# Optimization experiments

Measured on AMD Instinct MI355X. Metric: run time of the kernel, lower is better.

Reference implementation:

```python
import jax, jax.numpy as jnp
import numpy as np

D = 1024
H = 4096  # int(dim * mlp_ratio)
E = 8
B, N = 2, 2048


def setup_inputs() -> dict:
    key = jax.random.key(0)
    ks = jax.random.split(key, 5)
    x = jax.random.normal(ks[0], (B, N, D), dtype=jnp.float32)
    # torch Linear weights, stored pre-transposed for right-multiplication
    W1 = jax.random.normal(ks[1], (E, D, H), dtype=jnp.float32) / np.sqrt(D)
    W2 = jax.random.normal(ks[2], (E, H, D), dtype=jnp.float32) / np.sqrt(H)
    Wg = jax.random.normal(ks[3], (D, E), dtype=jnp.float32) / np.sqrt(D)
    bg = jax.random.normal(ks[4], (E,), dtype=jnp.float32) * 0.01
    return {"x": x, "W1": W1, "W2": W2, "Wg": Wg, "bg": bg}


def reference(x, W1, W2, Wg, bg):
    b, n, d = x.shape
    e = Wg.shape[1]
    xf = x.reshape(b * n, d)                      # [T, D]
    logits = xf @ Wg + bg                         # [T, E]
    one_hot = jax.nn.one_hot(jnp.argmax(logits, axis=-1), e, dtype=x.dtype)  # [T, E]
    # Dense all-experts compute (faithful to the original module)
    h = jax.nn.gelu(jnp.einsum('td,edh->eth', xf, W1), approximate=True)     # [E, T, H]
    y = jnp.einsum('eth,ehd->etd', h, W2)                                    # [E, T, D]
    out = jnp.einsum('etd,te->td', y, one_hot)                               # top-1 combine
    return out.reshape(b, n, d)
```

## Files before the change

kernel.cpp:

```cpp
#include <hip/hip_runtime.h>
#include <hip/hip_bf16.h>

#define Dq 1024
#define Hq 4096
#define Tq 4096
#define MAXTILES 40

#define XB_OFF 65536
#define HC_OFF (XB_OFF + Tq * Dq * 2)

#define M_NT 0
#define M_CNT 8
#define M_POFF 16
#define M_CUR 32
#define M_TE 64
#define M_TR 128
#define M_EXP 512
#define M_PERM 4608

typedef __attribute__((ext_vector_type(8))) short bf16x8;
typedef __attribute__((ext_vector_type(4))) float f32x4;

__device__ __forceinline__ short f2bf(float f) {
    __hip_bfloat16 h = __float2bfloat16(f);
    return *reinterpret_cast<short*>(&h);
}

__device__ __forceinline__ float gelu_tanh(float x) {
    float u = 0.7978845608028654f * (x + 0.044715f * x * x * x);
    return x / (1.0f + __expf(-2.0f * u));
}

typedef __attribute__((address_space(1))) const void gvoid;
typedef __attribute__((address_space(3))) void lvoid;
__device__ __forceinline__ void glds16(const void* g, void* l) {
    __builtin_amdgcn_global_load_lds((gvoid*)g, (lvoid*)l, 16, 0, 0);
}

#define WAITVM_(N) asm volatile("s_waitcnt vmcnt(" #N ")" ::: "memory")
#define WAITVM(N) WAITVM_(N)

__global__ void k_init(int* meta) {
    int i = blockIdx.x * 256 + threadIdx.x;
    if (i < M_PERM + MAXTILES * 128) meta[i] = 0;
}

__global__ void k_route(const float* __restrict__ x, const float* __restrict__ Wg,
                        const float* __restrict__ bg, int* meta, short* __restrict__ xb) {
    int wave = threadIdx.x >> 6;
    int lane = threadIdx.x & 63;
    int t = blockIdx.x * 4 + wave;
    const float* xr = x + (size_t)t * Dq;
    float acc[8];
#pragma unroll
    for (int e = 0; e < 8; ++e) acc[e] = 0.0f;
#pragma unroll
    for (int j = 0; j < 16; ++j) {
        int d = j * 64 + lane;
        float xv = xr[d];
        xb[(size_t)t * Dq + d] = f2bf(xv);
        float4 w0 = *(const float4*)(Wg + (size_t)d * 8);
        float4 w1 = *(const float4*)(Wg + (size_t)d * 8 + 4);
        acc[0] += xv * w0.x; acc[1] += xv * w0.y; acc[2] += xv * w0.z; acc[3] += xv * w0.w;
        acc[4] += xv * w1.x; acc[5] += xv * w1.y; acc[6] += xv * w1.z; acc[7] += xv * w1.w;
    }
#pragma unroll
    for (int e = 0; e < 8; ++e) {
#pragma unroll
        for (int off = 32; off > 0; off >>= 1) acc[e] += __shfl_xor(acc[e], off);
    }
    if (lane == 0) {
        float best = acc[0] + bg[0];
        int be = 0;
#pragma unroll
        for (int e = 1; e < 8; ++e) {
            float v = acc[e] + bg[e];
            if (v > best) { best = v; be = e; }
        }
        meta[M_EXP + t] = be;
        atomicAdd(&meta[M_CNT + be], 1);
    }
}

__global__ void k_scan(int* meta) {
    if (threadIdx.x != 0) return;
    int off = 0, nt = 0;
    for (int e = 0; e < 8; ++e) {
        meta[M_POFF + e] = off;
        int c = meta[M_CNT + e];
        int m = (c + 127) / 128;
        for (int j = 0; j < m; ++j) {
            meta[M_TE + nt] = e;
            meta[M_TR + nt] = off + j * 128;
            ++nt;
        }
        off += m * 128;
    }
    meta[M_POFF + 8] = off;
    meta[M_NT] = nt;
}

__global__ void k_scatter(int* meta) {
    int t = blockIdx.x * 256 + threadIdx.x;
    if (t >= Tq) return;
    int e = meta[M_EXP + t];
    int pos = atomicAdd(&meta[M_CUR + e], 1);
    meta[M_PERM + meta[M_POFF + e] + pos] = t;
}

#define STEP(RC, RN, P, ISS, KN, LDB)                                          \
  {                                                                            \
    if (ISS) {                                                                 \
      _Pragma("unroll")                                                        \
      for (int s = 0; s < 4; ++s)                                              \
        glds16(aSrc[s] + (size_t)(KN) * 64, As + (1 - (P)) * 8192 + ldsA[s]);  \
      _Pragma("unroll")                                                        \
      for (int r = 0; r < 8; ++r)                                              \
        RN[r] = *(const float4*)(bSrc + ((size_t)(KN) * 64 + r) * (LDB));      \
      WAITVM(12);                                                              \
    } else {                                                                   \
      WAITVM(0);                                                               \
    }                                                                          \
    _Pragma("unroll")                                                          \
    for (int j = 0; j < 4; ++j) {                                              \
      bf16x8 v;                                                                \
      _Pragma("unroll")                                                        \
      for (int r = 0; r < 8; ++r) v[r] = f2bf(((const float*)&RC[r])[j]);      \
      *(bf16x8*)(Bs + (P) * 8192 + bwoff[j]) = v;                              \
    }                                                                          \
    asm volatile("s_waitcnt lgkmcnt(0)" ::: "memory");                         \
    __builtin_amdgcn_s_barrier();                                              \
    asm volatile("" ::: "memory");                                             \
    __builtin_amdgcn_sched_barrier(0);                                         \
    _Pragma("unroll")                                                          \
    for (int s2 = 0; s2 < 2; ++s2) {                                           \
      bf16x8 af[4], bfv[4];                                                    \
      _Pragma("unroll")                                                        \
      for (int f = 0; f < 4; ++f) {                                            \
        af[f]  = *(const bf16x8*)(&As[(P) * 8192 + aoff[s2][f]]);              \
        bfv[f] = *(const bf16x8*)(&Bs[(P) * 8192 + boff[s2][f]]);              \
      }                                                                        \
      __builtin_amdgcn_s_setprio(1);                                           \
      _Pragma("unroll")                                                        \
      for (int fm = 0; fm < 4; ++fm)                                           \
        _Pragma("unroll")                                                      \
        for (int fn = 0; fn < 4; ++fn)                                         \
          acc[fm][fn] = __builtin_amdgcn_mfma_f32_16x16x32_bf16(               \
              af[fm], bfv[fn], acc[fm][fn], 0, 0, 0);                          \
      __builtin_amdgcn_s_setprio(0);                                           \
    }                                                                          \
    __builtin_amdgcn_s_barrier();                                              \
    asm volatile("" ::: "memory");                                             \
  }

#define GEMM_SETUP()                                                           \
    int tt = threadIdx.x, w = tt >> 6, lane = tt & 63;                         \
    int fr = lane & 15, fg = lane >> 4;                                        \
    int rlo = lane >> 3, csw = (lane & 7) ^ rlo;                               \
    int ldsA[4];                                                               \
    _Pragma("unroll")                                                          \
    for (int s = 0; s < 4; ++s) ldsA[s] = (s * 32 + w * 8) * 64;               \
    int n4 = (tt & 31) * 4, kb = (tt >> 5) * 8;                                \
    int bwoff[4];                                                              \
    _Pragma("unroll")                                                          \
    for (int j = 0; j < 4; ++j) {                                              \
      int n = n4 + j;                                                          \
      bwoff[j] = n * 64 + (((kb >> 3) ^ ((n + (n >> 3)) & 7)) * 8);            \
    }                                                                          \
    int wm = (w >> 1) * 64, wn = (w & 1) * 64;                                 \
    int aoff[2][4], boff[2][4];                                                \
    _Pragma("unroll")                                                          \
    for (int s2 = 0; s2 < 2; ++s2)                                             \
      _Pragma("unroll")                                                        \
      for (int f = 0; f < 4; ++f) {                                            \
        int c = s2 * 4 + fg;                                                   \
        int m = wm + f * 16 + fr;                                              \
        aoff[s2][f] = m * 64 + ((c ^ (m & 7)) * 8);                            \
        int n = wn + f * 16 + fr;                                              \
        boff[s2][f] = n * 64 + ((c ^ ((n + (n >> 3)) & 7)) * 8);               \
      }                                                                        \
    f32x4 acc[4][4];                                                           \
    _Pragma("unroll")                                                          \
    for (int a = 0; a < 4; ++a)                                                \
      _Pragma("unroll")                                                        \
      for (int b = 0; b < 4; ++b) acc[a][b] = (f32x4){0.f, 0.f, 0.f, 0.f};

__global__ __launch_bounds__(256, 2) void k_gemm1(const short* __restrict__ xb,
                                                  const float* __restrict__ W1,
                                                  const int* __restrict__ meta,
                                                  short* __restrict__ Hc) {
    __shared__ short As[2 * 128 * 64];
    __shared__ short Bs[2 * 128 * 64];
    int hw = blockIdx.x;
    int swzid = (hw & 7) * 160 + (hw >> 3);
    int q = swzid % 160;
    int mt = q >> 2;
    int n0 = ((swzid / 160) * 4 + (q & 3)) * 128;
    if (mt >= meta[M_NT]) return;
    int e = meta[M_TE + mt];
    int i0 = meta[M_TR + mt];
    const int* perm = meta + M_PERM;

    GEMM_SETUP()

    const short* aSrc[4];
#pragma unroll
    for (int s = 0; s < 4; ++s) {
        int row = s * 32 + w * 8 + rlo;
        aSrc[s] = xb + (size_t)perm[i0 + row] * Dq + csw * 8;
    }
    const float* bSrc = W1 + ((size_t)e * Dq + kb) * Hq + n0 + n4;

    float4 rB0[8], rB1[8];
#pragma unroll
    for (int s = 0; s < 4; ++s) glds16(aSrc[s], As + ldsA[s]);
#pragma unroll
    for (int r = 0; r < 8; ++r) rB0[r] = *(const float4*)(bSrc + (size_t)r * Hq);

    for (int t = 0; t < 16; t += 2) {
        STEP(rB0, rB1, 0, true, t + 1, Hq)
        STEP(rB1, rB0, 1, (t + 2) < 16, t + 2, Hq)
    }

#pragma unroll
    for (int fm = 0; fm < 4; ++fm) {
        int rbase = i0 + wm + fm * 16 + fg * 4;
#pragma unroll
        for (int fn = 0; fn < 4; ++fn) {
            int col = n0 + wn + fn * 16 + fr;
#pragma unroll
            for (int p = 0; p < 4; ++p) {
                float v = gelu_tanh(acc[fm][fn][p]);
                Hc[(size_t)(rbase + p) * Hq + col] = f2bf(v);
            }
        }
    }
}

__global__ __launch_bounds__(256, 2) void k_gemm2(const short* __restrict__ Hc,
                                                  const float* __restrict__ W2,
                                                  const int* __restrict__ meta,
                                                  float* __restrict__ out) {
    __shared__ short As[2 * 128 * 64];
    __shared__ short Bs[2 * 128 * 64];
    int hw = blockIdx.x;
    int swzid = (hw & 7) * 80 + (hw >> 3);
    int q = swzid % 80;
    int mt = q >> 1;
    int kbase = (q & 1) * (Hq / 2);
    int n0 = (swzid / 80) * 128;
    if (mt >= meta[M_NT]) return;
    int e = meta[M_TE + mt];
    int i0 = meta[M_TR + mt];
    const int* perm = meta + M_PERM;
    int vend = meta[M_POFF + e] + meta[M_CNT + e];

    GEMM_SETUP()

    const short* aSrc[4];
#pragma unroll
    for (int s = 0; s < 4; ++s) {
        int row = s * 32 + w * 8 + rlo;
        aSrc[s] = Hc + (size_t)(i0 + row) * Hq + kbase + csw * 8;
    }
    const float* bSrc = W2 + ((size_t)e * Hq + kbase + kb) * Dq + n0 + n4;

    float4 rB0[8], rB1[8];
#pragma unroll
    for (int s = 0; s < 4; ++s) glds16(aSrc[s], As + ldsA[s]);
#pragma unroll
    for (int r = 0; r < 8; ++r) rB0[r] = *(const float4*)(bSrc + (size_t)r * Dq);

    for (int t = 0; t < 32; t += 2) {
        STEP(rB0, rB1, 0, true, t + 1, Dq)
        STEP(rB1, rB0, 1, (t + 2) < 32, t + 2, Dq)
    }

#pragma unroll
    for (int fm = 0; fm < 4; ++fm) {
        int rbase = i0 + wm + fm * 16 + fg * 4;
#pragma unroll
        for (int p = 0; p < 4; ++p) {
            int i = rbase + p;
            if (i < vend) {
                int tok = perm[i];
#pragma unroll
                for (int fn = 0; fn < 4; ++fn) {
                    int col = n0 + wn + fn * 16 + fr;
                    atomicAdd(&out[(size_t)tok * Dq + col], acc[fm][fn][p]);
                }
            }
        }
    }
}

extern "C" void kernel_launch(void* const* d_in, const int* in_sizes, int n_in,
                              void* d_out, int out_size, void* d_ws, size_t ws_size,
                              hipStream_t stream) {
    const float* x  = (const float*)d_in[0];
    const float* W1 = (const float*)d_in[1];
    const float* W2 = (const float*)d_in[2];
    const float* Wg = (const float*)d_in[3];
    const float* bg = (const float*)d_in[4];
    float* out = (float*)d_out;
    int* meta = (int*)d_ws;
    short* xb = (short*)((char*)d_ws + XB_OFF);
    short* Hc = (short*)((char*)d_ws + HC_OFF);

    k_init<<<38, 256, 0, stream>>>(meta);
    hipMemsetAsync(d_out, 0, (size_t)Tq * Dq * 4, stream);
    k_route<<<Tq / 4, 256, 0, stream>>>(x, Wg, bg, meta, xb);
    k_scan<<<1, 64, 0, stream>>>(meta);
    k_scatter<<<Tq / 256, 256, 0, stream>>>(meta);
    k_gemm1<<<1280, 256, 0, stream>>>(xb, W1, meta, Hc);
    k_gemm2<<<640, 256, 0, stream>>>(Hc, W2, meta, out);
}
```

Before: 286.3 us.

## Pre-transpose weights to bf16 and load both GEMM operands directly to LDS

Adds a transpose kernel that converts W1 and W2 from fp32 into K-contiguous bf16 layouts in a workspace before each GEMM. Both GEMMs then fetch A and B through global-to-LDS loads with a single-buffered LDS and a simpler swizzle, dropping the in-register fp32-to-bf16 conversion of B. Occupancy hint rises to 3 and gemm2 switches to 4-way split-K over 1280 blocks. The transposes add a full extra pass over the weights each call, and the extra split-K increases atomic traffic to the output.

```diff
diff --git a/kernel.cpp b/kernel.cpp
--- a/kernel.cpp
+++ b/kernel.cpp
@@ -5,9 +5,11 @@
 #define Hq 4096
 #define Tq 4096
 #define MAXTILES 40
+#define NSTEP 16
 
 #define XB_OFF 65536
 #define HC_OFF (XB_OFF + Tq * Dq * 2)
+#define WT_OFF (HC_OFF + MAXTILES * 128 * Hq * 2)
 
 #define M_NT 0
 #define M_CNT 8
@@ -37,12 +39,36 @@
     __builtin_amdgcn_global_load_lds((gvoid*)g, (lvoid*)l, 16, 0, 0);
 }
 
-#define WAITVM_(N) asm volatile("s_waitcnt vmcnt(" #N ")" ::: "memory")
-#define WAITVM(N) WAITVM_(N)
-
 __global__ void k_init(int* meta) {
     int i = blockIdx.x * 256 + threadIdx.x;
     if (i < M_PERM + MAXTILES * 128) meta[i] = 0;
+}
+
+__global__ void k_tr(const float* __restrict__ in, short* __restrict__ out, int R, int C) {
+    __shared__ float t[64][65];
+    int e = blockIdx.z;
+    int c0 = blockIdx.x * 64;
+    int r0 = blockIdx.y * 64;
+    const float* ine = in + (size_t)e * R * C;
+    short* oute = out + (size_t)e * R * C;
+    int tt = threadIdx.x;
+    int lr = tt >> 4;
+    int lc = (tt & 15) * 4;
+#pragma unroll
+    for (int p = 0; p < 4; ++p) {
+        int r = p * 16 + lr;
+        float4 v = *(const float4*)(ine + (size_t)(r0 + r) * C + c0 + lc);
+        t[r][lc] = v.x; t[r][lc + 1] = v.y; t[r][lc + 2] = v.z; t[r][lc + 3] = v.w;
+    }
+    __syncthreads();
+#pragma unroll
+    for (int p = 0; p < 4; ++p) {
+        int c = p * 16 + lr;
+        short4 s;
+        s.x = f2bf(t[lc][c]); s.y = f2bf(t[lc + 1][c]);
+        s.z = f2bf(t[lc + 2][c]); s.w = f2bf(t[lc + 3][c]);
+        *(short4*)(oute + (size_t)(c0 + c) * R + r0 + lc) = s;
+    }
 }
 
 __global__ void k_route(const float* __restrict__ x, const float* __restrict__ Wg,
@@ -108,65 +134,14 @@
     meta[M_PERM + meta[M_POFF + e] + pos] = t;
 }
 
-#define STEP(RC, RN, P, ISS, KN, LDB)                                          \
-  {                                                                            \
-    if (ISS) {                                                                 \
-      _Pragma("unroll")                                                        \
-      for (int s = 0; s < 4; ++s)                                              \
-        glds16(aSrc[s] + (size_t)(KN) * 64, As + (1 - (P)) * 8192 + ldsA[s]);  \
-      _Pragma("unroll")                                                        \
-      for (int r = 0; r < 8; ++r)                                              \
-        RN[r] = *(const float4*)(bSrc + ((size_t)(KN) * 64 + r) * (LDB));      \
-      WAITVM(12);                                                              \
-    } else {                                                                   \
-      WAITVM(0);                                                               \
-    }                                                                          \
-    _Pragma("unroll")                                                          \
-    for (int j = 0; j < 4; ++j) {                                              \
-      bf16x8 v;                                                                \
-      _Pragma("unroll")                                                        \
-      for (int r = 0; r < 8; ++r) v[r] = f2bf(((const float*)&RC[r])[j]);      \
-      *(bf16x8*)(Bs + (P) * 8192 + bwoff[j]) = v;                              \
-    }                                                                          \
-    asm volatile("s_waitcnt lgkmcnt(0)" ::: "memory");                         \
-    __builtin_amdgcn_s_barrier();                                              \
-    asm volatile("" ::: "memory");                                             \
-    __builtin_amdgcn_sched_barrier(0);                                         \
-    _Pragma("unroll")                                                          \
-    for (int s2 = 0; s2 < 2; ++s2) {                                           \
-      bf16x8 af[4], bfv[4];                                                    \
-      _Pragma("unroll")                                                        \
-      for (int f = 0; f < 4; ++f) {                                            \
-        af[f]  = *(const bf16x8*)(&As[(P) * 8192 + aoff[s2][f]]);              \
-        bfv[f] = *(const bf16x8*)(&Bs[(P) * 8192 + boff[s2][f]]);              \
-      }                                                                        \
-      __builtin_amdgcn_s_setprio(1);                                           \
-      _Pragma("unroll")                                                        \
-      for (int fm = 0; fm < 4; ++fm)                                           \
-        _Pragma("unroll")                                                      \
-        for (int fn = 0; fn < 4; ++fn)                                         \
-          acc[fm][fn] = __builtin_amdgcn_mfma_f32_16x16x32_bf16(               \
-              af[fm], bfv[fn], acc[fm][fn], 0, 0, 0);                          \
-      __builtin_amdgcn_s_setprio(0);                                           \
-    }                                                                          \
-    __builtin_amdgcn_s_barrier();                                              \
-    asm volatile("" ::: "memory");                                             \
-  }
-
 #define GEMM_SETUP()                                                           \
     int tt = threadIdx.x, w = tt >> 6, lane = tt & 63;                         \
     int fr = lane & 15, fg = lane >> 4;                                        \
-    int rlo = lane >> 3, csw = (lane & 7) ^ rlo;                               \
-    int ldsA[4];                                                               \
-    _Pragma("unroll")                                                          \
-    for (int s = 0; s < 4; ++s) ldsA[s] = (s * 32 + w * 8) * 64;               \
-    int n4 = (tt & 31) * 4, kb = (tt >> 5) * 8;                                \
-    int bwoff[4];                                                              \
-    _Pragma("unroll")                                                          \
-    for (int j = 0; j < 4; ++j) {                                              \
-      int n = n4 + j;                                                          \
-      bwoff[j] = n * 64 + (((kb >> 3) ^ ((n + (n >> 3)) & 7)) * 8);            \
-    }                                                                          \
+    int rlo = lane >> 3;                                                       \
+    int csw = ((lane & 7) ^ rlo) * 8;                                          \
+    int ldsOff[4];                                                             \
+    _Pragma("unroll")                                                          \
+    for (int s = 0; s < 4; ++s) ldsOff[s] = (s * 32 + w * 8) * 64;             \
     int wm = (w >> 1) * 64, wn = (w & 1) * 64;                                 \
     int aoff[2][4], boff[2][4];                                                \
     _Pragma("unroll")                                                          \
@@ -177,7 +152,7 @@
         int m = wm + f * 16 + fr;                                              \
         aoff[s2][f] = m * 64 + ((c ^ (m & 7)) * 8);                            \
         int n = wn + f * 16 + fr;                                              \
-        boff[s2][f] = n * 64 + ((c ^ ((n + (n >> 3)) & 7)) * 8);               \
+        boff[s2][f] = n * 64 + ((c ^ (n & 7)) * 8);                            \
       }                                                                        \
     f32x4 acc[4][4];                                                           \
     _Pragma("unroll")                                                          \
@@ -185,17 +160,49 @@
       _Pragma("unroll")                                                        \
       for (int b = 0; b < 4; ++b) acc[a][b] = (f32x4){0.f, 0.f, 0.f, 0.f};
 
-__global__ __launch_bounds__(256, 2) void k_gemm1(const short* __restrict__ xb,
-                                                  const float* __restrict__ W1,
+#define KLOOP()                                                                \
+  _Pragma("unroll")                                                            \
+  for (int t = 0; t < NSTEP; ++t) {                                            \
+    __syncthreads();                                                           \
+    bf16x8 af[2][4], bv[2][4];                                                 \
+    _Pragma("unroll")                                                          \
+    for (int s2 = 0; s2 < 2; ++s2)                                             \
+      _Pragma("unroll")                                                        \
+      for (int f = 0; f < 4; ++f) {                                            \
+        af[s2][f] = *(const bf16x8*)(&As[aoff[s2][f]]);                        \
+        bv[s2][f] = *(const bf16x8*)(&Bs[boff[s2][f]]);                        \
+      }                                                                        \
+    __syncthreads();                                                           \
+    if (t + 1 < NSTEP) {                                                       \
+      _Pragma("unroll")                                                        \
+      for (int s = 0; s < 4; ++s) {                                            \
+        glds16(aSrc[s] + (t + 1) * 64, As + ldsOff[s]);                        \
+        glds16(bSrc[s] + (t + 1) * 64, Bs + ldsOff[s]);                        \
+      }                                                                        \
+    }                                                                          \
+    __builtin_amdgcn_sched_barrier(0);                                         \
+    __builtin_amdgcn_s_setprio(1);                                             \
+    _Pragma("unroll")                                                          \
+    for (int s2 = 0; s2 < 2; ++s2)                                             \
+      _Pragma("unroll")                                                        \
+      for (int fm = 0; fm < 4; ++fm)                                           \
+        _Pragma("unroll")                                                      \
+        for (int fn = 0; fn < 4; ++fn)                                         \
+          acc[fm][fn] = __builtin_amdgcn_mfma_f32_16x16x32_bf16(               \
+              af[s2][fm], bv[s2][fn], acc[fm][fn], 0, 0, 0);                   \
+    __builtin_amdgcn_s_setprio(0);                                             \
+  }
+
+__global__ __launch_bounds__(256, 3) void k_gemm1(const short* __restrict__ xb,
+                                                  const short* __restrict__ W1T,
                                                   const int* __restrict__ meta,
                                                   short* __restrict__ Hc) {
-    __shared__ short As[2 * 128 * 64];
-    __shared__ short Bs[2 * 128 * 64];
+    __shared__ short As[128 * 64];
+    __shared__ short Bs[128 * 64];
     int hw = blockIdx.x;
-    int swzid = (hw & 7) * 160 + (hw >> 3);
-    int q = swzid % 160;
+    int xcd = hw & 7, q = hw >> 3;
     int mt = q >> 2;
-    int n0 = ((swzid / 160) * 4 + (q & 3)) * 128;
+    int n0 = (xcd * 4 + (q & 3)) * 128;
     if (mt >= meta[M_NT]) return;
     int e = meta[M_TE + mt];
     int i0 = meta[M_TR + mt];
@@ -204,23 +211,21 @@
     GEMM_SETUP()
 
     const short* aSrc[4];
+    const short* bSrc[4];
 #pragma unroll
     for (int s = 0; s < 4; ++s) {
         int row = s * 32 + w * 8 + rlo;
-        aSrc[s] = xb + (size_t)perm[i0 + row] * Dq + csw * 8;
-    }
-    const float* bSrc = W1 + ((size_t)e * Dq + kb) * Hq + n0 + n4;
-
-    float4 rB0[8], rB1[8];
-#pragma unroll
-    for (int s = 0; s < 4; ++s) glds16(aSrc[s], As + ldsA[s]);
-#pragma unroll
-    for (int r = 0; r < 8; ++r) rB0[r] = *(const float4*)(bSrc + (size_t)r * Hq);
-
-    for (int t = 0; t < 16; t += 2) {
-        STEP(rB0, rB1, 0, true, t + 1, Hq)
-        STEP(rB1, rB0, 1, (t + 2) < 16, t + 2, Hq)
-    }
+        aSrc[s] = xb + (size_t)perm[i0 + row] * Dq + csw;
+        bSrc[s] = W1T + ((size_t)e * Hq + n0 + row) * Dq + csw;
+    }
+
+#pragma unroll
+    for (int s = 0; s < 4; ++s) {
+        glds16(aSrc[s], As + ldsOff[s]);
+        glds16(bSrc[s], Bs + ldsOff[s]);
+    }
+
+    KLOOP()
 
 #pragma unroll
     for (int fm = 0; fm < 4; ++fm) {
@@ -237,18 +242,18 @@
     }
 }
 
-__global__ __launch_bounds__(256, 2) void k_gemm2(const short* __restrict__ Hc,
-                                                  const float* __restrict__ W2,
+__global__ __launch_bounds__(256, 3) void k_gemm2(const short* __restrict__ Hc,
+                                                  const short* __restrict__ W2T,
                                                   const int* __restrict__ meta,
                                                   float* __restrict__ out) {
-    __shared__ short As[2 * 128 * 64];
-    __shared__ short Bs[2 * 128 * 64];
+    __shared__ short As[128 * 64];
+    __shared__ short Bs[128 * 64];
     int hw = blockIdx.x;
-    int swzid = (hw & 7) * 80 + (hw >> 3);
-    int q = swzid % 80;
-    int mt = q >> 1;
-    int kbase = (q & 1) * (Hq / 2);
-    int n0 = (swzid / 80) * 128;
+    int xcd = hw & 7, q = hw >> 3;
+    int mt = q >> 2;
+    int sk = q & 3;
+    int n0 = xcd * 128;
+    int kbase = sk * (Hq / 4);
     if (mt >= meta[M_NT]) return;
     int e = meta[M_TE + mt];
     int i0 = meta[M_TR + mt];
@@ -258,23 +263,21 @@
     GEMM_SETUP()
 
     const short* aSrc[4];
+    const short* bSrc[4];
 #pragma unroll
     for (int s = 0; s < 4; ++s) {
         int row = s * 32 + w * 8 + rlo;
-        aSrc[s] = Hc + (size_t)(i0 + row) * Hq + kbase + csw * 8;
-    }
-    const float* bSrc = W2 + ((size_t)e * Hq + kbase + kb) * Dq + n0 + n4;
-
-    float4 rB0[8], rB1[8];
-#pragma unroll
-    for (int s = 0; s < 4; ++s) glds16(aSrc[s], As + ldsA[s]);
-#pragma unroll
-    for (int r = 0; r < 8; ++r) rB0[r] = *(const float4*)(bSrc + (size_t)r * Dq);
-
-    for (int t = 0; t < 32; t += 2) {
-        STEP(rB0, rB1, 0, true, t + 1, Dq)
-        STEP(rB1, rB0, 1, (t + 2) < 32, t + 2, Dq)
-    }
+        aSrc[s] = Hc + (size_t)(i0 + row) * Hq + kbase + csw;
+        bSrc[s] = W2T + ((size_t)e * Dq + n0 + row) * Hq + kbase + csw;
+    }
+
+#pragma unroll
+    for (int s = 0; s < 4; ++s) {
+        glds16(aSrc[s], As + ldsOff[s]);
+        glds16(bSrc[s], Bs + ldsOff[s]);
+    }
+
+    KLOOP()
 
 #pragma unroll
     for (int fm = 0; fm < 4; ++fm) {
@@ -306,12 +309,15 @@
     int* meta = (int*)d_ws;
     short* xb = (short*)((char*)d_ws + XB_OFF);
     short* Hc = (short*)((char*)d_ws + HC_OFF);
+    short* WT = (short*)((char*)d_ws + WT_OFF);
 
     k_init<<<38, 256, 0, stream>>>(meta);
     hipMemsetAsync(d_out, 0, (size_t)Tq * Dq * 4, stream);
     k_route<<<Tq / 4, 256, 0, stream>>>(x, Wg, bg, meta, xb);
     k_scan<<<1, 64, 0, stream>>>(meta);
     k_scatter<<<Tq / 256, 256, 0, stream>>>(meta);
-    k_gemm1<<<1280, 256, 0, stream>>>(xb, W1, meta, Hc);
-    k_gemm2<<<640, 256, 0, stream>>>(Hc, W2, meta, out);
-}
+    k_tr<<<dim3(Hq / 64, Dq / 64, 8), 256, 0, stream>>>(W1, WT, Dq, Hq);
+    k_gemm1<<<1280, 256, 0, stream>>>(xb, WT, meta, Hc);
+    k_tr<<<dim3(Dq / 64, Hq / 64, 8), 256, 0, stream>>>(W2, WT, Hq, Dq);
+    k_gemm2<<<1280, 256, 0, stream>>>(Hc, WT, meta, out);
+}
```

Result: slower. 294.4 us (+2.8%).
